# Optimization experiments

Measured on AMD Instinct MI355X. Metric: run time of the kernel, lower is better.

Reference implementation:

```python
import jax, jax.numpy as jnp
import numpy as np

B, T, E = 2, 2048, 1024
H = 16
D = E // H  # head_dim = 64


def setup_inputs() -> dict:
    key = jax.random.key(0)
    ks = jax.random.split(key, 9)
    s = 1.0 / np.sqrt(E)
    inp = {"x": jax.random.normal(ks[0], (B, T, E), dtype=jnp.float32)}
    # Linear params (torch nn.Linear: y = x @ W.T + b)
    inp["Wq"] = jax.random.uniform(ks[1], (E, E), jnp.float32, -s, s)
    inp["bq"] = jax.random.uniform(ks[2], (E,), jnp.float32, -s, s)
    inp["Wk"] = jax.random.uniform(ks[3], (E, E), jnp.float32, -s, s)
    inp["bk"] = jax.random.uniform(ks[4], (E,), jnp.float32, -s, s)
    inp["Wv"] = jax.random.uniform(ks[5], (E, E), jnp.float32, -s, s)
    inp["bv"] = jax.random.uniform(ks[6], (E,), jnp.float32, -s, s)
    inp["Wo"] = jax.random.uniform(ks[7], (E, E), jnp.float32, -s, s)
    inp["bo"] = jax.random.uniform(ks[8], (E,), jnp.float32, -s, s)
    return inp


def reference(x, Wq, bq, Wk, bk, Wv, bv, Wo, bo):
    # QKV projections, reshape to [B, H, T, D]
    def split_heads(y):
        return y.reshape(B, T, H, D).transpose(0, 2, 1, 3)

    Q = split_heads(x @ Wq.T + bq)
    K = split_heads(x @ Wk.T + bk)
    V = split_heads(x @ Wv.T + bv)

    scale = 1.0 / jnp.sqrt(jnp.asarray(D, x.dtype))
    scores = jnp.einsum("bhqd,bhkd->bhqk", Q, K) * scale  # [B,H,T,T]
    attn = jax.nn.softmax(scores, axis=-1)
    out = jnp.einsum("bhqk,bhkd->bhqd", attn, V)  # [B,H,T,D]
    out = out.transpose(0, 2, 1, 3).reshape(B, T, E)
    # dropout is identity in eval mode
    return out @ Wo.T + bo
```

## Files before the change

### kernel.cpp

```cpp
#include <hip/hip_runtime.h>
#include <math.h>

#define BB 2
#define TT 2048
#define EE 1024
#define HH 16
#define DD 64
#define MM (BB*TT)
#define KK EE

typedef short bf16x8 __attribute__((ext_vector_type(8)));
typedef float f32x4  __attribute__((ext_vector_type(4)));

__device__ __forceinline__ unsigned short f2bf(float f) {
  unsigned int u = __float_as_uint(f);
  u = (u + 0x7FFFu + ((u >> 16) & 1u)) >> 16;
  return (unsigned short)u;
}

__device__ __forceinline__ void async16(const void* g, void* l) {
  __builtin_amdgcn_global_load_lds(
      (const __attribute__((address_space(1))) unsigned int*)g,
      (__attribute__((address_space(3))) unsigned int*)l, 16, 0, 0);
}

__global__ __launch_bounds__(256) void to_bf16(
    const float* __restrict__ x,  const float* __restrict__ wq,
    const float* __restrict__ wk, const float* __restrict__ wv,
    const float* __restrict__ wo,
    unsigned short* __restrict__ xh, unsigned short* __restrict__ wcat,
    unsigned short* __restrict__ woh)
{
  int c = blockIdx.x * 256 + threadIdx.x;
  const float* src; unsigned short* dst; int off;
  if (c < 1048576) { src = x; dst = xh; off = c; }
  else {
    int r = c - 1048576;
    int w = r >> 18;
    off = r & 262143;
    if      (w == 0) { src = wq; dst = wcat; }
    else if (w == 1) { src = wk; dst = wcat + (1 << 20); }
    else if (w == 2) { src = wv; dst = wcat + (2 << 20); }
    else             { src = wo; dst = woh; }
  }
  float4 v = ((const float4*)src)[off];
  ushort4 h;
  h.x = f2bf(v.x); h.y = f2bf(v.y); h.z = f2bf(v.z); h.w = f2bf(v.w);
  ((ushort4*)dst)[off] = h;
}

template<int MODE>
__global__ __launch_bounds__(256) void gemm_bf16(
    const unsigned short* __restrict__ A, const unsigned short* __restrict__ B,
    const float* __restrict__ b0p, const float* __restrict__ b1p,
    const float* __restrict__ b2p,
    unsigned short* __restrict__ oq, unsigned short* __restrict__ ok,
    unsigned short* __restrict__ ov, float* __restrict__ ofp, float qscale)
{
  __shared__ unsigned short As[128 * 32];
  __shared__ unsigned short Bs[128 * 32];

  const int tid  = threadIdx.x;
  const int lane = tid & 63;
  const int wv   = tid >> 6;
  const int col  = lane & 15;
  const int quad = lane >> 4;
  const int wm = (wv >> 1) * 64;
  const int wn = (wv & 1) * 64;
  const int m0 = blockIdx.x * 128;
  const int n0 = blockIdx.y * 128;

  const int srow = lane >> 2;
  const int sw16 = (((lane & 3) ^ ((lane >> 2) & 3)) << 3);
  const int fswA = ((quad ^ (col & 3)) << 3);

  f32x4 acc[4][4];
  const f32x4 z = {0.f, 0.f, 0.f, 0.f};
#pragma unroll
  for (int i = 0; i < 4; ++i)
#pragma unroll
    for (int j = 0; j < 4; ++j) acc[i][j] = z;

  for (int kt = 0; kt < KK; kt += 32) {
    __syncthreads();
#pragma unroll
    for (int s = 0; s < 4; ++s) {
      const int t = wv * 4 + s;
      const unsigned short* src; unsigned short* dst; int rb, g0;
      if (t < 8) { src = A; dst = As; rb = t * 16;       g0 = m0; }
      else       { src = B; dst = Bs; rb = (t - 8) * 16; g0 = n0; }
      async16(src + (size_t)(g0 + rb + srow) * KK + kt + sw16, dst + rb * 32);
    }
    __syncthreads();

    bf16x8 bf[4];
#pragma unroll
    for (int j = 0; j < 4; ++j)
      bf[j] = *(const bf16x8*)(Bs + (wn + j * 16 + col) * 32 + fswA);
#pragma unroll
    for (int i = 0; i < 4; ++i) {
      bf16x8 af = *(const bf16x8*)(As + (wm + i * 16 + col) * 32 + fswA);
#pragma unroll
      for (int j = 0; j < 4; ++j)
        acc[i][j] = __builtin_amdgcn_mfma_f32_16x16x32_bf16(af, bf[j], acc[i][j], 0, 0, 0);
    }
  }

  if (MODE == 0) {
    const int region = n0 >> 10;
    const float* bias = (region == 0) ? b0p : (region == 1) ? b1p : b2p;
    const float scl = (region == 0) ? qscale : 1.0f;
#pragma unroll
    for (int i = 0; i < 4; ++i) {
#pragma unroll
      for (int j = 0; j < 4; ++j) {
        const int n = n0 + wn + j * 16 + col;
        const int nl = n & 1023, h = nl >> 6, d = nl & 63;
        const float bs = bias[nl];
        const int mb = m0 + wm + i * 16 + quad * 4;
        const int b = mb >> 11, t = mb & (TT - 1);
        if (region < 2) {
          unsigned short* dst = (region == 0) ? oq : ok;
          unsigned short* row = dst + ((size_t)(b * HH + h) * TT + t) * DD + d;
#pragma unroll
          for (int r = 0; r < 4; ++r)
            row[(size_t)r * DD] = f2bf((acc[i][j][r] + bs) * scl);
        } else {
          ushort4 pk;
          pk.x = f2bf(acc[i][j][0] + bs);
          pk.y = f2bf(acc[i][j][1] + bs);
          pk.z = f2bf(acc[i][j][2] + bs);
          pk.w = f2bf(acc[i][j][3] + bs);
          *(ushort4*)(ov + ((size_t)(b * HH + h) * DD + d) * TT + t) = pk;
        }
      }
    }
  } else {
#pragma unroll
    for (int i = 0; i < 4; ++i) {
#pragma unroll
      for (int j = 0; j < 4; ++j) {
        const int n = n0 + wn + j * 16 + col;
        const float bs = b0p[n];
#pragma unroll
        for (int r = 0; r < 4; ++r) {
          const int m = m0 + wm + i * 16 + quad * 4 + r;
          ofp[(size_t)m * EE + n] = acc[i][j][r] + bs;
        }
      }
    }
  }
}

__global__ __launch_bounds__(256) void flash_mfma(
    const unsigned short* __restrict__ Qb, const unsigned short* __restrict__ Kb,
    const unsigned short* __restrict__ Vtb, unsigned short* __restrict__ ctx)
{
  __shared__ unsigned short QPs[128 * 72];
  __shared__ unsigned short Ks[2][64 * 64];
  __shared__ unsigned short Vts[2][64 * 64];

  const int tid  = threadIdx.x;
  const int lane = tid & 63;
  const int wv   = tid >> 6;
  const int col  = lane & 15;
  const int quad = lane >> 4;
  const int wm   = wv * 32;
  const int q0   = blockIdx.x * 128;
  const int bh   = blockIdx.y;

  const unsigned short* Qg = Qb  + (size_t)bh * TT * DD;
  const unsigned short* Kg = Kb  + (size_t)bh * TT * DD;
  const unsigned short* Vg = Vtb + (size_t)bh * DD * TT;

  const int srow = lane >> 3;
  const int sw16 = (((lane & 7) ^ ((lane >> 3) & 7)) << 3);
  const int cxor = (col & 7);

  auto stage_kv = [&](int kt, int b) {
#pragma unroll
    for (int s = 0; s < 4; ++s) {
      const int rb = (wv & 1) * 32 + s * 8;
      if (wv < 2)
        async16(Kg + (size_t)(kt + rb + srow) * DD + sw16, &Ks[b][rb * 64]);
      else
        async16(Vg + (size_t)(rb + srow) * TT + kt + sw16, &Vts[b][rb * 64]);
    }
  };

#pragma unroll
  for (int s = 0; s < 4; ++s) {
    const int rb = wv * 32 + s * 8;
    async16(Qg + (size_t)(q0 + rb + srow) * DD + sw16, &QPs[rb * 64]);
  }
  stage_kv(0, 0);
  __syncthreads();

  bf16x8 aq[2][2];
#pragma unroll
  for (int i = 0; i < 2; ++i)
#pragma unroll
    for (int h = 0; h < 2; ++h)
      aq[i][h] = *(const bf16x8*)(QPs + (wm + i * 16 + col) * 64 +
                                  (((h * 4 + quad) ^ cxor) << 3));
  __syncthreads();

  f32x4 o_acc[2][4];
  float lpart[2];
  const f32x4 z = {0.f, 0.f, 0.f, 0.f};
#pragma unroll
  for (int i = 0; i < 2; ++i) {
    lpart[i] = 0.f;
#pragma unroll
    for (int j = 0; j < 4; ++j) o_acc[i][j] = z;
  }

  for (int kt = 0; kt < TT; kt += 64) {
    const int buf = (kt >> 6) & 1;
    if (kt + 64 < TT) stage_kv(kt + 64, buf ^ 1);

    f32x4 sacc[2][4];
#pragma unroll
    for (int i = 0; i < 2; ++i)
#pragma unroll
      for (int j = 0; j < 4; ++j) sacc[i][j] = z;

#pragma unroll
    for (int j = 0; j < 4; ++j) {
      bf16x8 bk0 = *(const bf16x8*)(Ks[buf] + (j * 16 + col) * 64 + ((quad ^ cxor) << 3));
      bf16x8 bk1 = *(const bf16x8*)(Ks[buf] + (j * 16 + col) * 64 + (((4 + quad) ^ cxor) << 3));
#pragma unroll
      for (int i = 0; i < 2; ++i) {
        sacc[i][j] = __builtin_amdgcn_mfma_f32_16x16x32_bf16(bk0, aq[i][0], sacc[i][j], 0, 0, 0);
        sacc[i][j] = __builtin_amdgcn_mfma_f32_16x16x32_bf16(bk1, aq[i][1], sacc[i][j], 0, 0, 0);
      }
    }

#pragma unroll
    for (int i = 0; i < 2; ++i) {
      const int prow = (wm + i * 16 + col) * 72;
      float lp = 0.f;
#pragma unroll
      for (int j = 0; j < 4; ++j) {
        float p0 = __builtin_amdgcn_exp2f(sacc[i][j][0]);
        float p1 = __builtin_amdgcn_exp2f(sacc[i][j][1]);
        float p2 = __builtin_amdgcn_exp2f(sacc[i][j][2]);
        float p3 = __builtin_amdgcn_exp2f(sacc[i][j][3]);
        lp += (p0 + p1) + (p2 + p3);
        uint2 w;
        w.x = __builtin_amdgcn_perm(__float_as_uint(p1), __float_as_uint(p0), 0x07060302u);
        w.y = __builtin_amdgcn_perm(__float_as_uint(p3), __float_as_uint(p2), 0x07060302u);
        *(uint2*)(QPs + prow + j * 16 + quad * 4) = w;
      }
      lpart[i] += lp;
    }

    bf16x8 ap[2][2];
#pragma unroll
    for (int i = 0; i < 2; ++i) {
      ap[i][0] = *(const bf16x8*)(QPs + (wm + i * 16 + col) * 72 + quad * 8);
      ap[i][1] = *(const bf16x8*)(QPs + (wm + i * 16 + col) * 72 + 32 + quad * 8);
    }

#pragma unroll
    for (int j = 0; j < 4; ++j) {
      bf16x8 bv0 = *(const bf16x8*)(Vts[buf] + (j * 16 + col) * 64 + ((quad ^ cxor) << 3));
      bf16x8 bv1 = *(const bf16x8*)(Vts[buf] + (j * 16 + col) * 64 + (((4 + quad) ^ cxor) << 3));
#pragma unroll
      for (int i = 0; i < 2; ++i) {
        o_acc[i][j] = __builtin_amdgcn_mfma_f32_16x16x32_bf16(ap[i][0], bv0, o_acc[i][j], 0, 0, 0);
        o_acc[i][j] = __builtin_amdgcn_mfma_f32_16x16x32_bf16(ap[i][1], bv1, o_acc[i][j], 0, 0, 0);
      }
    }

    __syncthreads();
  }

  const int b = bh >> 4, h = bh & 15;
#pragma unroll
  for (int i = 0; i < 2; ++i) {
    float l = lpart[i];
    l += __shfl_xor(l, 16);
    l += __shfl_xor(l, 32);
#pragma unroll
    for (int r = 0; r < 4; ++r) {
      const float inv = 1.0f / __shfl(l, quad * 4 + r);
      const int t = q0 + wm + i * 16 + quad * 4 + r;
      const size_t base = ((size_t)(b * TT + t)) * EE + h * DD;
#pragma unroll
      for (int j = 0; j < 4; ++j)
        ctx[base + j * 16 + col] = f2bf(o_acc[i][j][r] * inv);
    }
  }
}

extern "C" void kernel_launch(void* const* d_in, const int* in_sizes, int n_in,
                              void* d_out, int out_size, void* d_ws, size_t ws_size,
                              hipStream_t stream) {
  const float* x  = (const float*)d_in[0];
  const float* Wq = (const float*)d_in[1];
  const float* bq = (const float*)d_in[2];
  const float* Wk = (const float*)d_in[3];
  const float* bk = (const float*)d_in[4];
  const float* Wv = (const float*)d_in[5];
  const float* bv = (const float*)d_in[6];
  const float* Wo = (const float*)d_in[7];
  const float* bo = (const float*)d_in[8];

  unsigned short* p = (unsigned short*)d_ws;
  const size_t XN = (size_t)MM * EE;
  const size_t WN = (size_t)EE * EE;
  unsigned short* x_h    = p;           p += XN;
  unsigned short* Wcat_h = p;           p += 3 * WN;
  unsigned short* Wo_h   = p;           p += WN;
  unsigned short* Qb     = p;           p += XN;
  unsigned short* Kb     = p;           p += XN;
  unsigned short* Vtb    = p;           p += XN;
  unsigned short* ctx_h  = x_h;

  to_bf16<<<8192, 256, 0, stream>>>(x, Wq, Wk, Wv, Wo, x_h, Wcat_h, Wo_h);

  const float qscale = 0.125f * 1.44269504088896f;

  gemm_bf16<0><<<dim3(MM / 128, 3 * EE / 128), 256, 0, stream>>>(
      x_h, Wcat_h, bq, bk, bv, Qb, Kb, Vtb, nullptr, qscale);

  flash_mfma<<<dim3(TT / 128, BB * HH), 256, 0, stream>>>(Qb, Kb, Vtb, ctx_h);

  gemm_bf16<2><<<dim3(MM / 128, EE / 128), 256, 0, stream>>>(
      ctx_h, Wo_h, bo, nullptr, nullptr,
      nullptr, nullptr, nullptr, (float*)d_out, 1.0f);
}
```

Before: 215.6 us.

## Stage GEMM and attention epilogues through LDS for coalesced 16-byte stores

```diff
diff --git a/kernel.cpp b/kernel.cpp
--- a/kernel.cpp
+++ b/kernel.cpp
@@ -57,8 +57,11 @@
     unsigned short* __restrict__ oq, unsigned short* __restrict__ ok,
     unsigned short* __restrict__ ov, float* __restrict__ ofp, float qscale)
 {
+  constexpr int NT = (MODE == 0) ? 128 : 64;
+  constexpr int JN = NT / 32;
   __shared__ unsigned short As[128 * 32];
   __shared__ unsigned short Bs[128 * 32];
+  __shared__ unsigned short Cs[(MODE == 0) ? 128 * 136 : 1];
 
   const int tid  = threadIdx.x;
   const int lane = tid & 63;
@@ -66,26 +69,27 @@
   const int col  = lane & 15;
   const int quad = lane >> 4;
   const int wm = (wv >> 1) * 64;
-  const int wn = (wv & 1) * 64;
+  const int wn = (wv & 1) * (NT / 2);
   const int m0 = blockIdx.x * 128;
-  const int n0 = blockIdx.y * 128;
+  const int n0 = blockIdx.y * NT;
 
   const int srow = lane >> 2;
   const int sw16 = (((lane & 3) ^ ((lane >> 2) & 3)) << 3);
   const int fswA = ((quad ^ (col & 3)) << 3);
 
-  f32x4 acc[4][4];
+  f32x4 acc[4][JN];
   const f32x4 z = {0.f, 0.f, 0.f, 0.f};
 #pragma unroll
   for (int i = 0; i < 4; ++i)
 #pragma unroll
-    for (int j = 0; j < 4; ++j) acc[i][j] = z;
-
+    for (int j = 0; j < JN; ++j) acc[i][j] = z;
+
+  constexpr int NW = (MODE == 0) ? 4 : 3;
   for (int kt = 0; kt < KK; kt += 32) {
     __syncthreads();
 #pragma unroll
-    for (int s = 0; s < 4; ++s) {
-      const int t = wv * 4 + s;
+    for (int s = 0; s < NW; ++s) {
+      const int t = wv * NW + s;
       const unsigned short* src; unsigned short* dst; int rb, g0;
       if (t < 8) { src = A; dst = As; rb = t * 16;       g0 = m0; }
       else       { src = B; dst = Bs; rb = (t - 8) * 16; g0 = n0; }
@@ -93,15 +97,15 @@
     }
     __syncthreads();
 
-    bf16x8 bf[4];
-#pragma unroll
-    for (int j = 0; j < 4; ++j)
+    bf16x8 bf[JN];
+#pragma unroll
+    for (int j = 0; j < JN; ++j)
       bf[j] = *(const bf16x8*)(Bs + (wn + j * 16 + col) * 32 + fswA);
 #pragma unroll
     for (int i = 0; i < 4; ++i) {
       bf16x8 af = *(const bf16x8*)(As + (wm + i * 16 + col) * 32 + fswA);
 #pragma unroll
-      for (int j = 0; j < 4; ++j)
+      for (int j = 0; j < JN; ++j)
         acc[i][j] = __builtin_amdgcn_mfma_f32_16x16x32_bf16(af, bf[j], acc[i][j], 0, 0, 0);
     }
   }
@@ -110,36 +114,60 @@
     const int region = n0 >> 10;
     const float* bias = (region == 0) ? b0p : (region == 1) ? b1p : b2p;
     const float scl = (region == 0) ? qscale : 1.0f;
-#pragma unroll
-    for (int i = 0; i < 4; ++i) {
-#pragma unroll
-      for (int j = 0; j < 4; ++j) {
-        const int n = n0 + wn + j * 16 + col;
-        const int nl = n & 1023, h = nl >> 6, d = nl & 63;
-        const float bs = bias[nl];
-        const int mb = m0 + wm + i * 16 + quad * 4;
-        const int b = mb >> 11, t = mb & (TT - 1);
-        if (region < 2) {
-          unsigned short* dst = (region == 0) ? oq : ok;
-          unsigned short* row = dst + ((size_t)(b * HH + h) * TT + t) * DD + d;
-#pragma unroll
-          for (int r = 0; r < 4; ++r)
-            row[(size_t)r * DD] = f2bf((acc[i][j][r] + bs) * scl);
-        } else {
+    const int nlbase = n0 & 1023;
+    const int h0 = nlbase >> 6;
+    const int b = m0 >> 11, t0 = m0 & (TT - 1);
+    if (region < 2) {
+#pragma unroll
+      for (int i = 0; i < 4; ++i)
+#pragma unroll
+        for (int j = 0; j < 4; ++j) {
+          const int nt = wn + j * 16 + col;
+          const float bs = bias[nlbase + nt];
+#pragma unroll
+          for (int r = 0; r < 4; ++r) {
+            const int mt = wm + i * 16 + quad * 4 + r;
+            Cs[mt * 136 + nt] = f2bf((acc[i][j][r] + bs) * scl);
+          }
+        }
+      __syncthreads();
+      unsigned short* dst = (region == 0) ? oq : ok;
+#pragma unroll
+      for (int s = 0; s < 8; ++s) {
+        const int u = s * 256 + tid;
+        const int mt = u >> 4, hs = (u >> 3) & 1, ch = u & 7;
+        const size_t g = ((size_t)(b * HH + h0 + hs) * TT + t0 + mt) * DD + ch * 8;
+        *(uint4*)(dst + g) = *(const uint4*)(Cs + mt * 136 + hs * 64 + ch * 8);
+      }
+    } else {
+#pragma unroll
+      for (int i = 0; i < 4; ++i)
+#pragma unroll
+        for (int j = 0; j < 4; ++j) {
+          const int nt = wn + j * 16 + col;
+          const float bs = bias[nlbase + nt];
           ushort4 pk;
           pk.x = f2bf(acc[i][j][0] + bs);
           pk.y = f2bf(acc[i][j][1] + bs);
           pk.z = f2bf(acc[i][j][2] + bs);
           pk.w = f2bf(acc[i][j][3] + bs);
-          *(ushort4*)(ov + ((size_t)(b * HH + h) * DD + d) * TT + t) = pk;
+          *(ushort4*)(Cs + nt * 136 + wm + i * 16 + quad * 4) = pk;
         }
+      __syncthreads();
+#pragma unroll
+      for (int s = 0; s < 8; ++s) {
+        const int u = s * 256 + tid;
+        const int nt = u >> 4, ch = u & 15;
+        const int d = nt & 63, hs = nt >> 6;
+        const size_t g = ((size_t)(b * HH + h0 + hs) * DD + d) * TT + t0 + ch * 8;
+        *(uint4*)(ov + g) = *(const uint4*)(Cs + nt * 136 + ch * 8);
       }
     }
   } else {
 #pragma unroll
     for (int i = 0; i < 4; ++i) {
 #pragma unroll
-      for (int j = 0; j < 4; ++j) {
+      for (int j = 0; j < JN; ++j) {
         const int n = n0 + wn + j * 16 + col;
         const float bs = b0p[n];
 #pragma unroll
@@ -276,6 +304,7 @@
     __syncthreads();
   }
 
+  unsigned short* Cs = &Ks[0][0];
   const int b = bh >> 4, h = bh & 15;
 #pragma unroll
   for (int i = 0; i < 2; ++i) {
@@ -285,12 +314,23 @@
 #pragma unroll
     for (int r = 0; r < 4; ++r) {
       const float inv = 1.0f / __shfl(l, quad * 4 + r);
-      const int t = q0 + wm + i * 16 + quad * 4 + r;
-      const size_t base = ((size_t)(b * TT + t)) * EE + h * DD;
-#pragma unroll
-      for (int j = 0; j < 4; ++j)
-        ctx[base + j * 16 + col] = f2bf(o_acc[i][j][r] * inv);
-    }
+      const int trow = wm + i * 16 + quad * 4 + r;
+#pragma unroll
+      for (int j = 0; j < 4; ++j) {
+        const int n = j * 16 + col;
+        const int ch = ((n >> 3) ^ (trow & 7)) << 3;
+        Cs[trow * 64 + ch + (n & 7)] = f2bf(o_acc[i][j][r] * inv);
+      }
+    }
+  }
+  __syncthreads();
+#pragma unroll
+  for (int s = 0; s < 4; ++s) {
+    const int u = s * 256 + tid;
+    const int mr = u >> 3, ch = u & 7;
+    const size_t g = ((size_t)(b * TT + q0 + mr)) * EE + h * DD + ch * 8;
+    const int chs = (ch ^ (mr & 7)) << 3;
+    *(uint4*)(ctx + g) = *(const uint4*)(Cs + mr * 64 + chs);
   }
 }
 
@@ -327,7 +367,7 @@
 
   flash_mfma<<<dim3(TT / 128, BB * HH), 256, 0, stream>>>(Qb, Kb, Vtb, ctx_h);
 
-  gemm_bf16<2><<<dim3(MM / 128, EE / 128), 256, 0, stream>>>(
+  gemm_bf16<2><<<dim3(MM / 128, EE / 64), 256, 0, stream>>>(
       ctx_h, Wo_h, bo, nullptr, nullptr,
       nullptr, nullptr, nullptr, (float*)d_out, 1.0f);
 }
```

Measured after the change: 209.7 us. -2.7%, faster.
